# Kernel tuning notes

Measured on AMD Instinct MI355X. Metric: run time of the kernel, lower is better.

Reference implementation:

```python
import jax, jax.numpy as jnp
import numpy as np

N_FFT = 2048
HOP = 441
WIN_SIZE = 7
PAD = WIN_SIZE // 2
NP_WIN = WIN_SIZE * WIN_SIZE
COV_NORM = NP_WIN / (NP_WIN - 1.0)  # sample covariance, skimage default
DATA_RANGE = 2.0  # skimage float dtype_range (-1,1)
C1 = (0.01 * DATA_RANGE) ** 2
C2 = (0.03 * DATA_RANGE) ** 2
EPS = 1e-8

# periodic hann window (librosa fftbins=True)
_HANN = 0.5 - 0.5 * np.cos(2.0 * np.pi * np.arange(N_FFT) / N_FFT)


def wav_to_spectrogram(x):
    # x: [B, C, S] -> magnitude spectrogram [B, C, T, F]
    pad = N_FFT // 2
    xp = jnp.pad(x, ((0, 0), (0, 0), (pad, pad)), mode='reflect')  # torch 'reflect'
    L = xp.shape[-1]
    n_frames = (L - N_FFT) // HOP + 1
    idx = jnp.arange(n_frames)[:, None] * HOP + jnp.arange(N_FFT)[None, :]
    frames = xp[..., idx] * jnp.asarray(_HANN, xp.dtype)  # [B,C,T,N_FFT]
    spec = jnp.fft.rfft(frames, axis=-1)
    mag = jnp.sqrt(jnp.maximum(spec.real ** 2 + spec.imag ** 2, EPS))
    return mag


def _umean_last(x):
    # 1D uniform mean filter (size 7) along last axis, scipy 'reflect' boundary
    xp = jnp.pad(x, [(0, 0)] * (x.ndim - 1) + [(PAD, PAD)], mode='symmetric')
    cs = jnp.cumsum(xp, axis=-1)
    zero = jnp.zeros(cs.shape[:-1] + (1,), cs.dtype)
    cs = jnp.concatenate([zero, cs], axis=-1)
    return (cs[..., WIN_SIZE:] - cs[..., :-WIN_SIZE]) / WIN_SIZE


def umean2d(x):
    # separable 7x7 uniform filter over last two axes
    x = _umean_last(x)
    x = jnp.swapaxes(_umean_last(jnp.swapaxes(x, -1, -2)), -1, -2)
    return x


def ssim_map_mean(X, Y):
    ux, uy = umean2d(X), umean2d(Y)
    uxx, uyy, uxy = umean2d(X * X), umean2d(Y * Y), umean2d(X * Y)
    vx = COV_NORM * (uxx - ux * ux)
    vy = COV_NORM * (uyy - uy * uy)
    vxy = COV_NORM * (uxy - ux * uy)
    S = ((2 * ux * uy + C1) * (2 * vxy + C2)) / ((ux * ux + uy * uy + C1) * (vx + vy + C2))
    # crop pad on each side (skimage) then mean over the spatial map
    return jnp.mean(S[..., PAD:-PAD, PAD:-PAD], axis=(-2, -1))


def setup_inputs() -> dict:
    key = jax.random.key(0)
    k1, k2 = jax.random.split(key)
    B, C, S = 32, 2, 176400
    output = jax.random.normal(k1, (B, C, S), dtype=jnp.float32)
    target = jax.random.normal(k2, (B, C, S), dtype=jnp.float32)
    return {"output": output, "target": target}


def reference(output, target):
    so = wav_to_spectrogram(output)
    st = wav_to_spectrogram(target)
    res = ssim_map_mean(so, st)  # [B, C]
    return res[..., None, None]  # [B, C, 1, 1]
```

## Files before the change

kernel.cpp:

```cpp
#include <hip/hip_runtime.h>
#include <math.h>

#ifndef M_PI
#define M_PI 3.14159265358979323846
#endif

constexpr int S_LEN    = 176400;
constexpr int NFFT     = 2048;
constexpr int NC       = 1024;
constexpr int HOP_     = 441;
constexpr int T_FRAMES = 401;
constexpr int F_BINS   = 1025;
constexpr int F_STRIDE = 1028;
constexpr int N_CH     = 64;
constexpr float EPS_   = 1e-8f;
constexpr float C1_    = 0.0004f;
constexpr float C2_    = 0.0036f;
constexpr float COV_NORM_ = 49.0f / 48.0f;

constexpr int WIN_OFF  = 0;
constexpr int TWG_OFF  = 2048;
constexpr int UTW_OFF  = 3584;
constexpr int SPEC_OFF = 5696;
constexpr int RPB_     = 10;
constexpr int N_CHUNKS = 40;

__device__ __forceinline__ int phys(int i) { return i ^ ((i >> 2) & 15); }

__device__ __forceinline__ float2 cadd(float2 a, float2 b){ return make_float2(a.x+b.x, a.y+b.y); }
__device__ __forceinline__ float2 csub(float2 a, float2 b){ return make_float2(a.x-b.x, a.y-b.y); }
__device__ __forceinline__ float2 cmul(float2 a, float2 b){ return make_float2(a.x*b.x-a.y*b.y, a.x*b.y+a.y*b.x); }

__global__ __launch_bounds__(256) void init_tables_kernel(float* __restrict__ ws, float* __restrict__ out) {
    const int idx = blockIdx.x * 256 + threadIdx.x;
    if (idx < 64) out[idx] = 0.0f;
    if (idx < NFFT) {
        ws[WIN_OFF + idx] = 0.5f - 0.5f * cosf((float)(2.0 * M_PI / NFFT) * (float)idx);
    }
    if (idx < 768) {
        float ang = -2.0f * (float)M_PI * (float)idx / (float)NC;
        float s, c; sincosf(ang, &s, &c);
        ws[TWG_OFF + 2*idx] = c; ws[TWG_OFF + 2*idx+1] = s;
    }
    if (idx < F_BINS) {
        float ang = -(float)M_PI * (float)idx / (float)NC;
        float s, c; sincosf(ang, &s, &c);
        ws[UTW_OFF + 2*idx] = c; ws[UTW_OFF + 2*idx+1] = s;
    }
}

__device__ __forceinline__ void r4_bfly(
    const float2* __restrict__ A, float2* __restrict__ B,
    int r0, int r1, int r2, int r3,
    int o0, int o1, int o2, int o3,
    float2 w1, float2 w2, float2 w3)
{
    float2 x0c = A[r0];
    float2 x1c = A[r1];
    float2 x2c = A[r2];
    float2 x3c = A[r3];

    float2 t0 = cadd(x0c, x2c);
    float2 t1 = csub(x0c, x2c);
    float2 t2 = cadd(x1c, x3c);
    float2 t3 = csub(x1c, x3c);

    float2 y0 = cadd(t0, t2);
    float2 y2 = csub(t0, t2);
    float2 y1 = make_float2(t1.x + t3.y, t1.y - t3.x);
    float2 y3 = make_float2(t1.x - t3.y, t1.y + t3.x);

    B[o0] = y0;
    B[o1] = cmul(y1, w1);
    B[o2] = cmul(y2, w2);
    B[o3] = cmul(y3, w3);
}

__global__ __launch_bounds__(256, 5) void stft_mag_kernel(
    const float* __restrict__ x0, const float* __restrict__ x1,
    float* __restrict__ ws, int ch0, int nch, int swizzle)
{
    __shared__ float2 bufA[2 * NC];
    __shared__ float2 bufB[2 * NC];

    const int tid = threadIdx.x;

    int ch, t;
    if (swizzle) {
        int g = blockIdx.x;
        ch = ch0 + (g & 7) * 8 + ((g >> 3) & 7);
        t  = g >> 6;
    } else {
        t  = blockIdx.x;
        ch = ch0 + blockIdx.y;
    }

    const float* __restrict__ xin0 = x0 + (size_t)ch * S_LEN;
    const float* __restrict__ xin1 = x1 + (size_t)ch * S_LEN;
    const float*  __restrict__ win = ws + WIN_OFF;
    const float2* __restrict__ twg = (const float2*)(ws + TWG_OFF);
    const float2* __restrict__ utw = (const float2*)(ws + UTW_OFF);

    const int base = t * HOP_ - NFFT / 2;
    float* fA0 = (float*)bufA;
    float* fA1 = (float*)(bufA + NC);
    if (base >= 0 && base + NFFT <= S_LEN) {
        #pragma unroll
        for (int k = 0; k < NFFT / 256; ++k) {
            int n = k * 256 + tid;
            int j = base + n;
            float w = win[n];
            int p = 2 * phys(n >> 1) + (n & 1);
            fA0[p] = xin0[j] * w;
            fA1[p] = xin1[j] * w;
        }
    } else {
        #pragma unroll
        for (int k = 0; k < NFFT / 256; ++k) {
            int n = k * 256 + tid;
            int j = base + n;
            j = (j < 0) ? -j : j;
            j = (j >= S_LEN) ? (2 * S_LEN - 2 - j) : j;
            float w = win[n];
            int p = 2 * phys(n >> 1) + (n & 1);
            fA0[p] = xin0[j] * w;
            fA1[p] = xin1[j] * w;
        }
    }
    __syncthreads();

    float2* A = bufA;
    float2* B = bufB;
    #pragma unroll
    for (int i = 0; i < 5; ++i) {
        const int s_ = 1 << (2 * i);
        const int q  = tid & (s_ - 1);
        const int ps = tid - q;

        const int r0 = phys(tid);
        const int r1 = phys(tid + 256);
        const int r2 = phys(tid + 512);
        const int r3 = phys(tid + 768);

        const float2 w1 = twg[ps];
        const float2 w2 = twg[2 * ps];
        const float2 w3 = twg[3 * ps];

        const int o  = q + 4 * ps;
        const int o0 = phys(o);
        const int o1 = phys(o + s_);
        const int o2 = phys(o + 2 * s_);
        const int o3 = phys(o + 3 * s_);

        r4_bfly(A,      B,      r0, r1, r2, r3, o0, o1, o2, o3, w1, w2, w3);
        r4_bfly(A + NC, B + NC, r0, r1, r2, r3, o0, o1, o2, o3, w1, w2, w3);

        __syncthreads();
        float2* tmp = A; A = B; B = tmp;
    }

    const size_t perT = (size_t)T_FRAMES * F_STRIDE;
    float* __restrict__ sout0 =
        ws + SPEC_OFF + (size_t)(ch - ch0) * perT + (size_t)t * F_STRIDE;
    float* __restrict__ sout1 = sout0 + (size_t)nch * perT;
    #pragma unroll
    for (int k = 0; k < 5; ++k) {
        int r = k * 256 + tid;
        if (k < 4 || tid == 0) {
            const int ra = phys(r & (NC - 1));
            const int rb = phys((NC - r) & (NC - 1));
            float2 wu = utw[r];

            {
                float2 Zr = A[ra];
                float2 Zn = A[rb];
                float Ex = 0.5f * (Zr.x + Zn.x);
                float Ey = 0.5f * (Zr.y - Zn.y);
                float Ox = 0.5f * (Zr.y + Zn.y);
                float Oy = 0.5f * (Zn.x - Zr.x);
                float Xx = Ex + wu.x * Ox - wu.y * Oy;
                float Xy = Ey + wu.x * Oy + wu.y * Ox;
                sout0[r] = sqrtf(fmaxf(Xx * Xx + Xy * Xy, EPS_));
            }
            {
                float2 Zr = A[NC + ra];
                float2 Zn = A[NC + rb];
                float Ex = 0.5f * (Zr.x + Zn.x);
                float Ey = 0.5f * (Zr.y - Zn.y);
                float Ox = 0.5f * (Zr.y + Zn.y);
                float Oy = 0.5f * (Zn.x - Zr.x);
                float Xx = Ex + wu.x * Ox - wu.y * Oy;
                float Xy = Ey + wu.x * Oy + wu.y * Ox;
                sout1[r] = sqrtf(fmaxf(Xx * Xx + Xy * Xy, EPS_));
            }
        }
    }
}

__global__ __launch_bounds__(256) void ssim_kernel(
    const float* __restrict__ ws, float* __restrict__ out,
    int ch0, int nch)
{
    __shared__ float csx[1284], csy[1284], csxx[1284], csyy[1284], csxy[1284];
    __shared__ double red[256];

    const int tid = threadIdx.x;
    const int cg  = blockIdx.y;
    const int ch  = ch0 + cg;
    const float* __restrict__ spec = ws + SPEC_OFF;
    const size_t per_ch = (size_t)T_FRAMES * F_STRIDE;
    const float* __restrict__ X = spec + (size_t)cg * per_ch;
    const float* __restrict__ Y = spec + ((size_t)nch + cg) * per_ch;

    const int t_begin = 3 + blockIdx.x * RPB_;
    const int t_end_  = min(t_begin + RPB_, T_FRAMES - 3);

    const int fv = tid << 2;
    const bool last = (tid == 255);
    const float inv49 = 1.0f / 49.0f;
    double acc = 0.0;

    float sx[4] = {0,0,0,0}, sy[4] = {0,0,0,0}, sxx[4] = {0,0,0,0},
          syy[4] = {0,0,0,0}, sxy[4] = {0,0,0,0};
    float s5[5] = {0,0,0,0,0};

    for (int rr = t_begin - 3; rr < t_begin + 3; ++rr) {
        float4 xv = *(const float4*)(X + (size_t)rr * F_STRIDE + fv);
        float4 yv = *(const float4*)(Y + (size_t)rr * F_STRIDE + fv);
        float xa[4] = {xv.x, xv.y, xv.z, xv.w}, ya[4] = {yv.x, yv.y, yv.z, yv.w};
        #pragma unroll
        for (int c = 0; c < 4; ++c) {
            sx[c] += xa[c]; sy[c] += ya[c];
            sxx[c] += xa[c]*xa[c]; syy[c] += ya[c]*ya[c]; sxy[c] += xa[c]*ya[c];
        }
        if (last) {
            float xe = X[(size_t)rr * F_STRIDE + 1024];
            float ye = Y[(size_t)rr * F_STRIDE + 1024];
            s5[0] += xe; s5[1] += ye; s5[2] += xe*xe; s5[3] += ye*ye; s5[4] += xe*ye;
        }
    }

    float4 ax, ay, bx, by; float a5x=0, a5y=0, b5x=0, b5y=0;
    ax = *(const float4*)(X + (size_t)(t_begin + 3) * F_STRIDE + fv);
    ay = *(const float4*)(Y + (size_t)(t_begin + 3) * F_STRIDE + fv);
    bx = *(const float4*)(X + (size_t)(t_begin - 3) * F_STRIDE + fv);
    by = *(const float4*)(Y + (size_t)(t_begin - 3) * F_STRIDE + fv);
    if (last) {
        a5x = X[(size_t)(t_begin + 3) * F_STRIDE + 1024];
        a5y = Y[(size_t)(t_begin + 3) * F_STRIDE + 1024];
        b5x = X[(size_t)(t_begin - 3) * F_STRIDE + 1024];
        b5y = Y[(size_t)(t_begin - 3) * F_STRIDE + 1024];
    }

    const int fo = 3 + (tid << 2);

    for (int t = t_begin; t < t_end_; ++t) {
        {
            float xa[4] = {ax.x, ax.y, ax.z, ax.w}, ya[4] = {ay.x, ay.y, ay.z, ay.w};
            #pragma unroll
            for (int c = 0; c < 4; ++c) {
                sx[c] += xa[c]; sy[c] += ya[c];
                sxx[c] += xa[c]*xa[c]; syy[c] += ya[c]*ya[c]; sxy[c] += xa[c]*ya[c];
                int p = 5 * tid + c;
                csx[p] = sx[c]; csy[p] = sy[c];
                csxx[p] = sxx[c]; csyy[p] = syy[c]; csxy[p] = sxy[c];
            }
            if (last) {
                s5[0] += a5x; s5[1] += a5y; s5[2] += a5x*a5x; s5[3] += a5y*a5y; s5[4] += a5x*a5y;
                csx[1280] = s5[0]; csy[1280] = s5[1];
                csxx[1280] = s5[2]; csyy[1280] = s5[3]; csxy[1280] = s5[4];
            }
        }
        __syncthreads();

        {
            float xa[4] = {bx.x, bx.y, bx.z, bx.w}, ya[4] = {by.x, by.y, by.z, by.w};
            #pragma unroll
            for (int c = 0; c < 4; ++c) {
                sx[c] -= xa[c]; sy[c] -= ya[c];
                sxx[c] -= xa[c]*xa[c]; syy[c] -= ya[c]*ya[c]; sxy[c] -= xa[c]*ya[c];
            }
            if (last) {
                s5[0] -= b5x; s5[1] -= b5y; s5[2] -= b5x*b5x; s5[3] -= b5y*b5y; s5[4] -= b5x*b5y;
            }
        }
        if (t + 1 < t_end_) {
            ax = *(const float4*)(X + (size_t)(t + 4) * F_STRIDE + fv);
            ay = *(const float4*)(Y + (size_t)(t + 4) * F_STRIDE + fv);
            bx = *(const float4*)(X + (size_t)(t - 2) * F_STRIDE + fv);
            by = *(const float4*)(Y + (size_t)(t - 2) * F_STRIDE + fv);
            if (last) {
                a5x = X[(size_t)(t + 4) * F_STRIDE + 1024];
                a5y = Y[(size_t)(t + 4) * F_STRIDE + 1024];
                b5x = X[(size_t)(t - 2) * F_STRIDE + 1024];
                b5y = Y[(size_t)(t - 2) * F_STRIDE + 1024];
            }
        }

        if (tid < 255) {
            float tx[10], ty[10], txx[10], tyy[10], txy[10];
            #pragma unroll
            for (int d = 0; d < 10; ++d) {
                int p = 5 * tid + d + (d >> 2);
                tx[d] = csx[p]; ty[d] = csy[p];
                txx[d] = csxx[p]; tyy[d] = csyy[p]; txy[d] = csxy[p];
            }
            float wx  = tx[0]+tx[1]+tx[2]+tx[3]+tx[4]+tx[5]+tx[6];
            float wy  = ty[0]+ty[1]+ty[2]+ty[3]+ty[4]+ty[5]+ty[6];
            float wxx = txx[0]+txx[1]+txx[2]+txx[3]+txx[4]+txx[5]+txx[6];
            float wyy = tyy[0]+tyy[1]+tyy[2]+tyy[3]+tyy[4]+tyy[5]+tyy[6];
            float wxy = txy[0]+txy[1]+txy[2]+txy[3]+txy[4]+txy[5]+txy[6];
            #pragma unroll
            for (int c = 0; c < 4; ++c) {
                if (fo + c <= 1021) {
                    float ux  = wx * inv49, uy  = wy * inv49;
                    float uxx = wxx * inv49, uyy = wyy * inv49, uxy = wxy * inv49;
                    float vx  = COV_NORM_ * (uxx - ux * ux);
                    float vy  = COV_NORM_ * (uyy - uy * uy);
                    float vxy = COV_NORM_ * (uxy - ux * uy);
                    float Sv = ((2.f * ux * uy + C1_) * (2.f * vxy + C2_)) /
                               ((ux * ux + uy * uy + C1_) * (vx + vy + C2_));
                    acc += (double)Sv;
                }
                if (c < 3) {
                    wx  += tx[c+7]  - tx[c];
                    wy  += ty[c+7]  - ty[c];
                    wxx += txx[c+7] - txx[c];
                    wyy += tyy[c+7] - tyy[c];
                    wxy += txy[c+7] - txy[c];
                }
            }
        }
        __syncthreads();
    }

    red[tid] = acc;
    __syncthreads();
    for (int off = 128; off > 0; off >>= 1) {
        if (tid < off) red[tid] += red[tid + off];
        __syncthreads();
    }
    if (tid == 0) {
        atomicAdd(&out[ch], (float)(red[0] / (395.0 * 1019.0)));
    }
}

extern "C" void kernel_launch(void* const* d_in, const int* in_sizes, int n_in,
                              void* d_out, int out_size, void* d_ws, size_t ws_size,
                              hipStream_t stream) {
    const float* x0 = (const float*)d_in[0];
    const float* x1 = (const float*)d_in[1];
    float* out = (float*)d_out;
    float* ws  = (float*)d_ws;

    const size_t table_bytes  = (size_t)SPEC_OFF * sizeof(float);
    const size_t per_ch_bytes = (size_t)2 * T_FRAMES * F_STRIDE * sizeof(float);
    int G = (int)((ws_size - table_bytes) / per_ch_bytes);
    if (G > N_CH) G = N_CH;
    if (G < 1)    G = 1;

    init_tables_kernel<<<dim3(16), dim3(256), 0, stream>>>(ws, out);

    for (int ch0 = 0; ch0 < N_CH; ch0 += G) {
        const int nch = (N_CH - ch0 < G) ? (N_CH - ch0) : G;

        if (nch == 64) {
            stft_mag_kernel<<<dim3(T_FRAMES * 64), dim3(256), 0, stream>>>(x0, x1, ws, ch0, nch, 1);
        } else {
            stft_mag_kernel<<<dim3(T_FRAMES, nch), dim3(256), 0, stream>>>(x0, x1, ws, ch0, nch, 0);
        }

        dim3 g2(N_CHUNKS, nch);
        ssim_kernel<<<g2, 256, 0, stream>>>(ws, out, ch0, nch);
    }
}
```

Measured before the change: 365.3 us.

## Switch STFT FFT to in-place radix-4 DIF with digit-reversed readout

Replaces the out-of-place Stockham radix-4 FFT, which ping-ponged between two shared buffers, with an in-place decimation-in-frequency FFT that uses a single shared buffer. The last stage skips twiddle multiplies, and the real-FFT post-processing reads the output in base-4 digit-reversed order. Halving shared memory per block allows the launch-bounds occupancy hint to rise from 5 to 8 blocks, aiming to hide global load and store latency. The swizzle gains an extra XOR term to limit bank conflicts at the new strides, but the in-place access pattern and bit-reversed reads may still cause LDS conflicts or scattered access.

```diff
diff --git a/kernel.cpp b/kernel.cpp
--- a/kernel.cpp
+++ b/kernel.cpp
@@ -25,7 +25,7 @@
 constexpr int RPB_     = 10;
 constexpr int N_CHUNKS = 40;
 
-__device__ __forceinline__ int phys(int i) { return i ^ ((i >> 2) & 15); }
+__device__ __forceinline__ int phys(int i) { return i ^ ((i >> 2) & 15) ^ ((i >> 6) & 15); }
 
 __device__ __forceinline__ float2 cadd(float2 a, float2 b){ return make_float2(a.x+b.x, a.y+b.y); }
 __device__ __forceinline__ float2 csub(float2 a, float2 b){ return make_float2(a.x-b.x, a.y-b.y); }
@@ -49,39 +49,36 @@
     }
 }
 
-__device__ __forceinline__ void r4_bfly(
-    const float2* __restrict__ A, float2* __restrict__ B,
-    int r0, int r1, int r2, int r3,
-    int o0, int o1, int o2, int o3,
-    float2 w1, float2 w2, float2 w3)
+__device__ __forceinline__ void r4_dif_inplace(
+    float2* __restrict__ A, int r0, int r1, int r2, int r3,
+    float2 w1, float2 w2, float2 w3, bool tw)
 {
     float2 x0c = A[r0];
     float2 x1c = A[r1];
     float2 x2c = A[r2];
     float2 x3c = A[r3];
 
-    float2 t0 = cadd(x0c, x2c);
-    float2 t1 = csub(x0c, x2c);
-    float2 t2 = cadd(x1c, x3c);
-    float2 t3 = csub(x1c, x3c);
-
-    float2 y0 = cadd(t0, t2);
-    float2 y2 = csub(t0, t2);
-    float2 y1 = make_float2(t1.x + t3.y, t1.y - t3.x);
-    float2 y3 = make_float2(t1.x - t3.y, t1.y + t3.x);
-
-    B[o0] = y0;
-    B[o1] = cmul(y1, w1);
-    B[o2] = cmul(y2, w2);
-    B[o3] = cmul(y3, w3);
-}
-
-__global__ __launch_bounds__(256, 5) void stft_mag_kernel(
+    float2 a = cadd(x0c, x2c);
+    float2 b = csub(x0c, x2c);
+    float2 c = cadd(x1c, x3c);
+    float2 d = csub(x1c, x3c);
+
+    float2 y0 = cadd(a, c);
+    float2 y2 = csub(a, c);
+    float2 y1 = make_float2(b.x + d.y, b.y - d.x);
+    float2 y3 = make_float2(b.x - d.y, b.y + d.x);
+
+    A[r0] = y0;
+    A[r1] = tw ? cmul(y1, w1) : y1;
+    A[r2] = tw ? cmul(y2, w2) : y2;
+    A[r3] = tw ? cmul(y3, w3) : y3;
+}
+
+__global__ __launch_bounds__(256, 8) void stft_mag_kernel(
     const float* __restrict__ x0, const float* __restrict__ x1,
     float* __restrict__ ws, int ch0, int nch, int swizzle)
 {
-    __shared__ float2 bufA[2 * NC];
-    __shared__ float2 bufB[2 * NC];
+    __shared__ float2 buf[2 * NC];
 
     const int tid = threadIdx.x;
 
@@ -102,8 +99,8 @@
     const float2* __restrict__ utw = (const float2*)(ws + UTW_OFF);
 
     const int base = t * HOP_ - NFFT / 2;
-    float* fA0 = (float*)bufA;
-    float* fA1 = (float*)(bufA + NC);
+    float* fA0 = (float*)buf;
+    float* fA1 = (float*)(buf + NC);
     if (base >= 0 && base + NFFT <= S_LEN) {
         #pragma unroll
         for (int k = 0; k < NFFT / 256; ++k) {
@@ -129,51 +126,55 @@
     }
     __syncthreads();
 
-    float2* A = bufA;
-    float2* B = bufB;
     #pragma unroll
-    for (int i = 0; i < 5; ++i) {
-        const int s_ = 1 << (2 * i);
-        const int q  = tid & (s_ - 1);
-        const int ps = tid - q;
-
-        const int r0 = phys(tid);
-        const int r1 = phys(tid + 256);
-        const int r2 = phys(tid + 512);
-        const int r3 = phys(tid + 768);
-
-        const float2 w1 = twg[ps];
-        const float2 w2 = twg[2 * ps];
-        const float2 w3 = twg[3 * ps];
-
-        const int o  = q + 4 * ps;
-        const int o0 = phys(o);
-        const int o1 = phys(o + s_);
-        const int o2 = phys(o + 2 * s_);
-        const int o3 = phys(o + 3 * s_);
-
-        r4_bfly(A,      B,      r0, r1, r2, r3, o0, o1, o2, o3, w1, w2, w3);
-        r4_bfly(A + NC, B + NC, r0, r1, r2, r3, o0, o1, o2, o3, w1, w2, w3);
+    for (int s = 0; s < 5; ++s) {
+        const int M  = 256 >> (2 * s);
+        const int q  = tid & (M - 1);
+        const int e  = q << (2 * s);
+        const int i0 = 4 * (tid - q) + q;
+
+        const int r0 = phys(i0);
+        const int r1 = phys(i0 + M);
+        const int r2 = phys(i0 + 2 * M);
+        const int r3 = phys(i0 + 3 * M);
+
+        float2 w1, w2, w3;
+        if (s < 4) {
+            w1 = twg[e];
+            w2 = twg[2 * e];
+            w3 = twg[3 * e];
+        } else {
+            w1 = w2 = w3 = make_float2(1.0f, 0.0f);
+        }
+
+        r4_dif_inplace(buf,      r0, r1, r2, r3, w1, w2, w3, s < 4);
+        r4_dif_inplace(buf + NC, r0, r1, r2, r3, w1, w2, w3, s < 4);
 
         __syncthreads();
-        float2* tmp = A; A = B; B = tmp;
     }
 
     const size_t perT = (size_t)T_FRAMES * F_STRIDE;
     float* __restrict__ sout0 =
         ws + SPEC_OFF + (size_t)(ch - ch0) * perT + (size_t)t * F_STRIDE;
     float* __restrict__ sout1 = sout0 + (size_t)nch * perT;
+
+    const int R8 = ((tid & 3) << 6) | ((tid & 12) << 2) | ((tid >> 2) & 12) | ((tid >> 6) & 3);
+
     #pragma unroll
     for (int k = 0; k < 5; ++k) {
         int r = k * 256 + tid;
         if (k < 4 || tid == 0) {
-            const int ra = phys(r & (NC - 1));
-            const int rb = phys((NC - r) & (NC - 1));
+            const int ra = (k < 4) ? ((R8 << 2) | k) : 0;
+            const int rn = (NC - r) & (NC - 1);
+            const int rb = ((rn & 3) << 8) | ((rn & 12) << 4) | (rn & 48)
+                         | ((rn >> 4) & 12) | ((rn >> 8) & 3);
+            const int ia = phys(ra);
+            const int ib = phys(rb);
             float2 wu = utw[r];
 
             {
-                float2 Zr = A[ra];
-                float2 Zn = A[rb];
+                float2 Zr = buf[ia];
+                float2 Zn = buf[ib];
                 float Ex = 0.5f * (Zr.x + Zn.x);
                 float Ey = 0.5f * (Zr.y - Zn.y);
                 float Ox = 0.5f * (Zr.y + Zn.y);
@@ -183,8 +184,8 @@
                 sout0[r] = sqrtf(fmaxf(Xx * Xx + Xy * Xy, EPS_));
             }
             {
-                float2 Zr = A[NC + ra];
-                float2 Zn = A[NC + rb];
+                float2 Zr = buf[NC + ia];
+                float2 Zn = buf[NC + ib];
                 float Ex = 0.5f * (Zr.x + Zn.x);
                 float Ey = 0.5f * (Zr.y - Zn.y);
                 float Ox = 0.5f * (Zr.y + Zn.y);
```

Measured after the change: 342.0 us. 1.07x faster.
